# Kernel optimization log

Measured on AMD Instinct MI355X. Metric: run time of the kernel, lower is better.

The kernel has to match this reference:

```python
import jax, jax.numpy as jnp
import numpy as np

B, N = 256, 256


def greedy_hard_perm(soft_perm):
    # soft_perm: (B, N, N). Sequential greedy masked-argmax assignment, vectorized over batch.
    Bn, Nn, _ = soft_perm.shape
    NEG = jnp.finfo(soft_perm.dtype).min
    b_idx = jnp.arange(Bn)

    def step(carry, _):
        scores, hard, row_mask, col_mask = carry
        # mask out already-assigned rows/cols (in-place masked_fill_ in torch -> carried scores)
        scores = jnp.where(row_mask[:, :, None], NEG, scores)
        scores = jnp.where(col_mask[:, None, :], NEG, scores)
        flat_idx = jnp.argmax(scores.reshape(Bn, -1), axis=1)  # (B,)
        r = flat_idx // Nn
        c = flat_idx % Nn
        hard = hard.at[b_idx, r, c].set(1.0)
        row_mask = row_mask.at[b_idx, r].set(True)
        col_mask = col_mask.at[b_idx, c].set(True)
        return (scores, hard, row_mask, col_mask), None

    init = (
        soft_perm,
        jnp.zeros_like(soft_perm),
        jnp.zeros((Bn, Nn), dtype=bool),
        jnp.zeros((Bn, Nn), dtype=bool),
    )
    (_, hard, _, _), _ = jax.lax.scan(step, init, None, length=Nn)
    return hard


def setup_inputs() -> dict:
    key = jax.random.key(0)
    logits = jax.random.normal(key, (B, N, N), dtype=jnp.float32)
    # realistic soft permutation: row-stochastic scores
    soft_perm = jax.nn.softmax(logits, axis=-1)
    return {"soft_perm": soft_perm}


def reference(soft_perm):
    # hard perm carries no gradient (built from constant 1.0 writes in torch)
    hard = greedy_hard_perm(jax.lax.stop_gradient(soft_perm))
    # straight-through estimator: forward = hard, backward = identity through soft
    return hard + soft_perm - jax.lax.stop_gradient(soft_perm)
```

## Files before the change

### kernel.cpp

```cpp
#include <hip/hip_runtime.h>
#include <math.h>

#define NEGINF (-INFINITY)
#define NEGINF_BITS ((int)0xFF800000)

typedef unsigned int u32;
typedef unsigned long long u64;

#define RST 128

__device__ __forceinline__ int rl_i(int x, int l) {
    return __builtin_amdgcn_readlane(x, l);
}
__device__ __forceinline__ float rl_f(float x, int l) {
    return __int_as_float(__builtin_amdgcn_readlane(__float_as_int(x), l));
}

__device__ __forceinline__ int wave_argmax_flat(float v, int f) {
#define AIX(CTRL) {                                                            \
        float vin = __int_as_float(__builtin_amdgcn_update_dpp(                \
            __float_as_int(v), __float_as_int(v), CTRL, 0xf, 0xf, false));     \
        int fin = __builtin_amdgcn_update_dpp(f, f, CTRL, 0xf, 0xf, false);    \
        const bool c = vin >= v;                                               \
        v = c ? vin : v;                                                       \
        f = c ? fin : f; }
    AIX(0x111) AIX(0x112) AIX(0x114) AIX(0x118) AIX(0x142) AIX(0x143)
#undef AIX
    return rl_i(f, 63);
}

__device__ __forceinline__ void wave_top2(float lv, int lf, float lv2, int lf2,
                                          float& nv, int& nc, float& nv2, int& nc2) {
    float av = lv, bv = lv2;
#define T2STAGE(CTRL) {                                                        \
        float a2 = __int_as_float(__builtin_amdgcn_update_dpp(                 \
            NEGINF_BITS, __float_as_int(av), CTRL, 0xf, 0xf, false));          \
        float b2 = __int_as_float(__builtin_amdgcn_update_dpp(                 \
            NEGINF_BITS, __float_as_int(bv), CTRL, 0xf, 0xf, false));          \
        float t = fminf(av, a2);                                               \
        av = fmaxf(av, a2);                                                    \
        bv = fmaxf(fmaxf(bv, b2), t); }
    T2STAGE(0x111) T2STAGE(0x112) T2STAGE(0x114) T2STAGE(0x118)
    T2STAGE(0x142) T2STAGE(0x143)
#undef T2STAGE
    nv = rl_f(av, 63);
    float sv = rl_f(bv, 63);

    u64 m1 = __ballot(lv == nv);
    int ln = (int)__builtin_ctzll(m1);
    nc = rl_i(lf, ln);

    nv2 = sv; nc2 = 300;
    if (sv > 0.f) {
        if (sv == nv) {
            float b2v = rl_f(lv2, ln);
            if (b2v == nv) {
                nc2 = rl_i(lf2, ln);
            } else {
                u64 rest = m1 & (m1 - 1);
                int l2 = (int)__builtin_ctzll(rest);
                nc2 = rl_i(lf, l2);
            }
        } else {
            u64 m2 = __ballot(lv == sv || lv2 == sv);
            int l2 = (int)__builtin_ctzll(m2);
            float tl = rl_f(lv, l2);
            nc2 = (tl == sv) ? rl_i(lf, l2) : rl_i(lf2, l2);
        }
    }
}

template <int RSTT>
__global__ __launch_bounds__(64, 1) void greedy_perm_kernel(
        const float* __restrict__ soft, float* __restrict__ out) {
    extern __shared__ float smem[];
    const int b = blockIdx.x;
    const int lane = threadIdx.x;
    const size_t base = (size_t)b << 16;
    const float* sc = soft + base;
    float* ob = out + base;

    float rv[4], spv[4];
    int   rc[4], spc[4];
#pragma unroll
    for (int j = 0; j < 4; ++j) { rv[j] = NEGINF; rc[j] = 0; spv[j] = NEGINF; spc[j] = 300; }

    const float4 zero4 = make_float4(0.f, 0.f, 0.f, 0.f);

    for (int k = 0; k < 64; k += 4) {
        float4 w[4][4];
#pragma unroll
        for (int j = 0; j < 4; ++j) {
            const float4* rp = (const float4*)(sc + (size_t)(4 * lane + j) * 256);
#pragma unroll
            for (int kk = 0; kk < 4; ++kk) w[j][kk] = rp[k + kk];
        }
#pragma unroll
        for (int j = 0; j < 4; ++j) {
            float4* op = (float4*)(ob + (size_t)(4 * lane + j) * 256);
#pragma unroll
            for (int kk = 0; kk < 4; ++kk) op[k + kk] = zero4;
        }
        if (RSTT > 0 && lane < (RSTT >> 2)) {
#pragma unroll
            for (int j = 0; j < 4; ++j) {
                float* lp = &smem[(4 * lane + j) << 8];
#pragma unroll
                for (int kk = 0; kk < 4; ++kk)
                    *(float4*)&lp[(((k + kk) ^ lane) & 63) << 2] = w[j][kk];
            }
        }
#pragma unroll
        for (int j = 0; j < 4; ++j) {
#pragma unroll
            for (int kk = 0; kk < 4; ++kk) {
                const float4 ww = w[j][kk];
                const int bc = 4 * (k + kk);
                const float e[4] = {ww.x, ww.y, ww.z, ww.w};
#pragma unroll
                for (int q = 0; q < 4; ++q) {
                    const float x = e[q];
                    const int   cx = bc + q;
                    const bool g1 = x > rv[j];
                    const bool g2 = x > spv[j];
                    spv[j] = g1 ? rv[j] : (g2 ? x  : spv[j]);
                    spc[j] = g1 ? rc[j] : (g2 ? cx : spc[j]);
                    rv[j]  = g1 ? x  : rv[j];
                    rc[j]  = g1 ? cx : rc[j];
                }
            }
        }
    }

    __threadfence_block();

    u32 colmask = 0;

    for (int step = 0; step < 256; ++step) {
        float bv = rv[0];
        int   bf = (lane << 10) | (rc[0] & 255);
#pragma unroll
        for (int j = 1; j < 4; ++j) {
            if (rv[j] > bv) { bv = rv[j]; bf = (lane << 10) | (j << 8) | (rc[j] & 255); }
        }
        const int gf = wave_argmax_flat(bv, bf);
        const int cc    = gf & 255;
        const int owner = gf >> 10;
        const int rj    = (gf >> 8) & 3;

        if (lane == 0) ob[gf] = 1.0f;
        if (lane == (cc >> 2)) colmask |= 1u << (cc & 3);
        const bool iown = (lane == owner);

        u32 needmask = 0;
#pragma unroll
        for (int j = 0; j < 4; ++j) {
            if (spc[j] == cc) spc[j] = 300;
            const bool match = (rc[j] == cc);
            if (match) {
                const bool win  = iown && (j == rj);
                const bool have = (spc[j] < 300);
                if (win) {
                    rv[j] = NEGINF; rc[j] = 300;
                } else if (have) {
                    rv[j] = spv[j]; rc[j] = spc[j];
                    spv[j] = NEGINF; spc[j] = 300;
                } else {
                    needmask |= 1u << j;
                }
            }
        }

        u64 nb = __ballot(needmask != 0);
        while (nb) {
            const int l = (int)__builtin_ctzll(nb); nb &= nb - 1;
            u32 nm = (u32)rl_i((int)needmask, l);
            while (nm) {
                const int j = (int)__builtin_ctzll(nm); nm &= nm - 1;
                const int row = (l << 2) + j;
                float4 w = (RSTT > 0 && row < RSTT)
                    ? *(const float4*)&smem[(row << 8) | (((lane ^ l) & 63) << 2)]
                    : *(const float4*)(sc + ((size_t)row << 8) + (lane << 2));
                const float q0 = (colmask & 1u) ? NEGINF : w.x;
                const float q1 = (colmask & 2u) ? NEGINF : w.y;
                const float q2 = (colmask & 4u) ? NEGINF : w.z;
                const float q3 = (colmask & 8u) ? NEGINF : w.w;
                const int cb = lane << 2;
                float lv = q0; int lf = cb;
                float lv2 = NEGINF; int lf2 = cb;
                {
                    bool g1 = q1 > lv, g2 = q1 > lv2;
                    lv2 = g1 ? lv : (g2 ? q1 : lv2); lf2 = g1 ? lf : (g2 ? cb + 1 : lf2);
                    lv  = g1 ? q1 : lv;              lf  = g1 ? cb + 1 : lf;
                    g1 = q2 > lv; g2 = q2 > lv2;
                    lv2 = g1 ? lv : (g2 ? q2 : lv2); lf2 = g1 ? lf : (g2 ? cb + 2 : lf2);
                    lv  = g1 ? q2 : lv;              lf  = g1 ? cb + 2 : lf;
                    g1 = q3 > lv; g2 = q3 > lv2;
                    lv2 = g1 ? lv : (g2 ? q3 : lv2); lf2 = g1 ? lf : (g2 ? cb + 3 : lf2);
                    lv  = g1 ? q3 : lv;              lf  = g1 ? cb + 3 : lf;
                }
                float fv, fv2; int fc, fc2;
                wave_top2(lv, lf, lv2, lf2, fv, fc, fv2, fc2);
                if (lane == l) {
#pragma unroll
                    for (int jj = 0; jj < 4; ++jj) if (jj == j) {
                        rv[jj] = fv; rc[jj] = fc;
                        spv[jj] = fv2; spc[jj] = fc2;
                    }
                }
            }
        }
    }
}

extern "C" void kernel_launch(void* const* d_in, const int* in_sizes, int n_in,
                              void* d_out, int out_size, void* d_ws, size_t ws_size,
                              hipStream_t stream) {
    const float* soft = (const float*)d_in[0];
    float* out = (float*)d_out;
    const int n_batches = in_sizes[0] >> 16;

    hipError_t e = hipFuncSetAttribute(
        reinterpret_cast<const void*>(greedy_perm_kernel<RST>),
        hipFuncAttributeMaxDynamicSharedMemorySize, RST * 256 * 4);
    if (e == hipSuccess)
        greedy_perm_kernel<RST><<<n_batches, 64, RST * 256 * 4, stream>>>(soft, out);
    else
        greedy_perm_kernel<0><<<n_batches, 64, 0, stream>>>(soft, out);
}
```

Baseline: 322.0 us.

## Interleave row ownership across lanes and defer one-hot writes to the end

Rows are now owned as j*64+lane instead of 4*lane+j, so each lane's column loads and zero stores stride across rows differently. The LDS row cache is filled by all lanes for the first two row groups. The per-step wave argmax becomes a max reduction, a ballot, and a lowest-index tie-break loop instead of the carried-index DPP argmax. Each step's scattered single-lane store of 1.0 is replaced by recording the assigned column per row in registers and writing them all once after the loop. This removes a global store from the serial critical path, at the cost of an extra ballot and possible tie loop per step.

```diff
diff --git a/kernel.cpp b/kernel.cpp
--- a/kernel.cpp
+++ b/kernel.cpp
@@ -16,17 +16,37 @@
     return __int_as_float(__builtin_amdgcn_readlane(__float_as_int(x), l));
 }
 
-__device__ __forceinline__ int wave_argmax_flat(float v, int f) {
-#define AIX(CTRL) {                                                            \
-        float vin = __int_as_float(__builtin_amdgcn_update_dpp(                \
-            __float_as_int(v), __float_as_int(v), CTRL, 0xf, 0xf, false));     \
-        int fin = __builtin_amdgcn_update_dpp(f, f, CTRL, 0xf, 0xf, false);    \
-        const bool c = vin >= v;                                               \
-        v = c ? vin : v;                                                       \
-        f = c ? fin : f; }
-    AIX(0x111) AIX(0x112) AIX(0x114) AIX(0x118) AIX(0x142) AIX(0x143)
-#undef AIX
-    return rl_i(f, 63);
+template <int CTRL>
+__device__ __forceinline__ float dppmax(float x) {
+    int xi = __float_as_int(x);
+    int yi = __builtin_amdgcn_update_dpp(xi, xi, CTRL, 0xf, 0xf, false);
+    return fmaxf(x, __int_as_float(yi));
+}
+
+__device__ __forceinline__ float wave_max64(float x) {
+    x = dppmax<0x111>(x);
+    x = dppmax<0x112>(x);
+    x = dppmax<0x114>(x);
+    x = dppmax<0x118>(x);
+    x = dppmax<0x142>(x);
+    x = dppmax<0x143>(x);
+    return rl_f(x, 63);
+}
+
+__device__ __forceinline__ void wave_argmax(float v, int idx, float& out_v, int& out_idx) {
+    float mv = wave_max64(v);
+    u64 mask = __ballot(v == mv);
+    int ln = (int)__builtin_ctzll(mask);
+    int bi = rl_i(idx, ln);
+    u64 rest = mask & (mask - 1);
+    if (rest) {
+        while (rest) {
+            int l2 = (int)__builtin_ctzll(rest); rest &= rest - 1;
+            int b2 = rl_i(idx, l2);
+            if (b2 < bi) bi = b2;
+        }
+    }
+    out_v = mv; out_idx = bi;
 }
 
 __device__ __forceinline__ void wave_top2(float lv, int lf, float lv2, int lf2,
@@ -81,9 +101,11 @@
     float* ob = out + base;
 
     float rv[4], spv[4];
-    int   rc[4], spc[4];
-#pragma unroll
-    for (int j = 0; j < 4; ++j) { rv[j] = NEGINF; rc[j] = 0; spv[j] = NEGINF; spc[j] = 300; }
+    int   rc[4], spc[4], acol[4];
+#pragma unroll
+    for (int j = 0; j < 4; ++j) {
+        rv[j] = NEGINF; rc[j] = 0; spv[j] = NEGINF; spc[j] = 300; acol[j] = 0;
+    }
 
     const float4 zero4 = make_float4(0.f, 0.f, 0.f, 0.f);
 
@@ -91,23 +113,23 @@
         float4 w[4][4];
 #pragma unroll
         for (int j = 0; j < 4; ++j) {
-            const float4* rp = (const float4*)(sc + (size_t)(4 * lane + j) * 256);
+            const float4* rp = (const float4*)(sc + (size_t)(j * 64 + lane) * 256);
 #pragma unroll
             for (int kk = 0; kk < 4; ++kk) w[j][kk] = rp[k + kk];
         }
 #pragma unroll
         for (int j = 0; j < 4; ++j) {
-            float4* op = (float4*)(ob + (size_t)(4 * lane + j) * 256);
+            float4* op = (float4*)(ob + (size_t)(j * 64 + lane) * 256);
 #pragma unroll
             for (int kk = 0; kk < 4; ++kk) op[k + kk] = zero4;
         }
-        if (RSTT > 0 && lane < (RSTT >> 2)) {
-#pragma unroll
-            for (int j = 0; j < 4; ++j) {
-                float* lp = &smem[(4 * lane + j) << 8];
+        if (RSTT > 0) {
+#pragma unroll
+            for (int j = 0; j < 2; ++j) {
+                float* lp = &smem[(j * 64 + lane) << 8];
 #pragma unroll
                 for (int kk = 0; kk < 4; ++kk)
-                    *(float4*)&lp[(((k + kk) ^ lane) & 63) << 2] = w[j][kk];
+                    *(float4*)&lp[((k + kk) ^ lane) << 2] = w[j][kk];
             }
         }
 #pragma unroll
@@ -138,31 +160,29 @@
 
     for (int step = 0; step < 256; ++step) {
         float bv = rv[0];
-        int   bf = (lane << 10) | (rc[0] & 255);
+        int   bf = (lane << 8) | (rc[0] & 255);
 #pragma unroll
         for (int j = 1; j < 4; ++j) {
-            if (rv[j] > bv) { bv = rv[j]; bf = (lane << 10) | (j << 8) | (rc[j] & 255); }
-        }
-        const int gf = wave_argmax_flat(bv, bf);
-        const int cc    = gf & 255;
-        const int owner = gf >> 10;
-        const int rj    = (gf >> 8) & 3;
-
-        if (lane == 0) ob[gf] = 1.0f;
+            if (rv[j] > bv) { bv = rv[j]; bf = (((j << 6) + lane) << 8) | (rc[j] & 255); }
+        }
+        float gv; int gf;
+        wave_argmax(bv, bf, gv, gf);
+        (void)gv;
+        const int r  = gf >> 8;
+        const int cc = gf & 255;
+
         if (lane == (cc >> 2)) colmask |= 1u << (cc & 3);
-        const bool iown = (lane == owner);
+        const bool iown = (lane == (r & 63));
+        const int  rj   = r >> 6;
 
         u32 needmask = 0;
 #pragma unroll
         for (int j = 0; j < 4; ++j) {
             if (spc[j] == cc) spc[j] = 300;
-            const bool match = (rc[j] == cc);
-            if (match) {
-                const bool win  = iown && (j == rj);
-                const bool have = (spc[j] < 300);
-                if (win) {
-                    rv[j] = NEGINF; rc[j] = 300;
-                } else if (have) {
+            if (rc[j] == cc) {
+                if (iown && j == rj) {
+                    rv[j] = NEGINF; rc[j] = 300; acol[j] = cc;
+                } else if (spc[j] < 300) {
                     rv[j] = spv[j]; rc[j] = spc[j];
                     spv[j] = NEGINF; spc[j] = 300;
                 } else {
@@ -177,7 +197,7 @@
             u32 nm = (u32)rl_i((int)needmask, l);
             while (nm) {
                 const int j = (int)__builtin_ctzll(nm); nm &= nm - 1;
-                const int row = (l << 2) + j;
+                const int row = (j << 6) + l;
                 float4 w = (RSTT > 0 && row < RSTT)
                     ? *(const float4*)&smem[(row << 8) | (((lane ^ l) & 63) << 2)]
                     : *(const float4*)(sc + ((size_t)row << 8) + (lane << 2));
@@ -211,6 +231,10 @@
             }
         }
     }
+
+#pragma unroll
+    for (int j = 0; j < 4; ++j)
+        ob[(size_t)(j * 64 + lane) * 256 + acol[j]] = 1.0f;
 }
 
 extern "C" void kernel_launch(void* const* d_in, const int* in_sizes, int n_in,
```

After: 313.7 us. -2.6%, faster.
